# Kernel optimization log

Measured on AMD Instinct MI355X. Metric: run time of the kernel, lower is better.

## Reference

```python
import jax, jax.numpy as jnp
import numpy as np

TEMPERATURE = 8.0  # sqrt(d_k), d_k = 64
MINIMUM_VALUE = -1e9  # stand-in for C.MINIMUM_VALUE


def setup_inputs() -> dict:
    key = jax.random.key(0)
    kq, kk, kv, km = jax.random.split(key, 4)
    B, N, D = 32, 2048, 64
    q = jax.random.normal(kq, (B, N, D), dtype=jnp.float32)
    k = jax.random.normal(kk, (B, N, D), dtype=jnp.float32)
    v = jax.random.normal(kv, (B, N, D), dtype=jnp.float32)
    mask = jax.random.randint(km, (B, N, N), 0, 2, dtype=jnp.int32)
    return {"q": q, "k": k, "v": v, "mask": mask}


def reference(q, k, v, mask):
    # scores: [B, Nq, Nk]
    attn = jnp.einsum("bqd,bkd->bqk", q, k) / TEMPERATURE
    attn = jnp.where(mask > 0, attn, MINIMUM_VALUE)
    attn = jax.nn.softmax(attn, axis=-1)
    # dropout is identity in eval / deterministic reference
    output = jnp.einsum("bqk,bkd->bqd", attn, v)
    return (output, attn)
```

## Files before the change

### kernel.cpp

```cpp
#include <hip/hip_runtime.h>

#define NB 32
#define NN 2048
#define ND 64
#define ROWS 16
#define NBLK (NB * NN / ROWS)

#define LDS_PART 65536
#define LDS_TOTAL 66048

typedef _Float16 half8 __attribute__((ext_vector_type(8)));
typedef float f32x4 __attribute__((ext_vector_type(4)));
typedef int i32x4 __attribute__((ext_vector_type(4)));

union H4 { uint2 u; _Float16 h[4]; };

__device__ __forceinline__ f32x4 mfma16(half8 a, half8 b, f32x4 c) {
    return __builtin_amdgcn_mfma_f32_16x16x32_f16(a, b, c, 0, 0, 0);
}
#define SB() __builtin_amdgcn_sched_barrier(0)
#define LBAR() { asm volatile("s_waitcnt lgkmcnt(0)" ::: "memory"); \
                 __builtin_amdgcn_s_barrier(); \
                 __builtin_amdgcn_sched_barrier(0); }

__global__ __launch_bounds__(256) void cvt_f32_f16_k(const float* __restrict__ src,
                                                     _Float16* __restrict__ dst) {
    int i = blockIdx.x * 256 + threadIdx.x;
    const f32x4* s = (const f32x4*)src;
    f32x4 a = s[2 * i], b = s[2 * i + 1];
    half8 h;
    h[0] = (_Float16)a[0]; h[1] = (_Float16)a[1]; h[2] = (_Float16)a[2]; h[3] = (_Float16)a[3];
    h[4] = (_Float16)b[0]; h[5] = (_Float16)b[1]; h[6] = (_Float16)b[2]; h[7] = (_Float16)b[3];
    ((half8*)dst)[i] = h;
}

__global__ __launch_bounds__(256) void transpose_v_k(const float* __restrict__ v,
                                                     _Float16* __restrict__ vt) {
    __shared__ float tile[64][65];
    int b = blockIdx.x >> 5;
    int k0 = (blockIdx.x & 31) * 64;
    int t = threadIdx.x;
    {
        int dc = t & 15, kr = t >> 4;
        const f32x4* vp = (const f32x4*)(v + ((size_t)(b * NN + k0) * ND));
        #pragma unroll
        for (int i = 0; i < 4; ++i) {
            int kk = kr + i * 16;
            f32x4 x = vp[kk * 16 + dc];
            tile[kk][dc * 4 + 0] = x[0]; tile[kk][dc * 4 + 1] = x[1];
            tile[kk][dc * 4 + 2] = x[2]; tile[kk][dc * 4 + 3] = x[3];
        }
    }
    __syncthreads();
    {
        int d = t >> 2, ks = (t & 3) * 16;
        union { _Float16 hh[16]; uint4 u4[2]; } pk;
        #pragma unroll
        for (int j = 0; j < 16; ++j) pk.hh[j] = (_Float16)tile[ks + j][d];
        uint4* op = (uint4*)(vt + ((size_t)(b * ND + d) * NN + k0 + ks));
        op[0] = pk.u4[0]; op[1] = pk.u4[1];
    }
}

__global__ __launch_bounds__(256) void mask_pack_k(const int* __restrict__ mask,
                                                   unsigned long long* __restrict__ pm) {
    size_t gid = (size_t)blockIdx.x * 256 + threadIdx.x;
    size_t row = gid >> 5;
    int w = ((int)gid >> 2) & 7, lg = (int)gid & 3;
    const i32x4* mp = (const i32x4*)(mask + row * NN + w * 16 + lg * 4);
    unsigned long long bits = 0ull;
    #pragma unroll
    for (int i = 0; i < 16; i += 4) {
        i32x4 m0 = __builtin_nontemporal_load(mp + (size_t)(i + 0) * 32);
        i32x4 m1 = __builtin_nontemporal_load(mp + (size_t)(i + 1) * 32);
        i32x4 m2 = __builtin_nontemporal_load(mp + (size_t)(i + 2) * 32);
        i32x4 m3 = __builtin_nontemporal_load(mp + (size_t)(i + 3) * 32);
        unsigned b0 = (m0[0] > 0 ? 1u : 0u) | (m0[1] > 0 ? 2u : 0u) | (m0[2] > 0 ? 4u : 0u) | (m0[3] > 0 ? 8u : 0u);
        unsigned b1 = (m1[0] > 0 ? 1u : 0u) | (m1[1] > 0 ? 2u : 0u) | (m1[2] > 0 ? 4u : 0u) | (m1[3] > 0 ? 8u : 0u);
        unsigned b2 = (m2[0] > 0 ? 1u : 0u) | (m2[1] > 0 ? 2u : 0u) | (m2[2] > 0 ? 4u : 0u) | (m2[3] > 0 ? 8u : 0u);
        unsigned b3 = (m3[0] > 0 ? 1u : 0u) | (m3[1] > 0 ? 2u : 0u) | (m3[2] > 0 ? 4u : 0u) | (m3[3] > 0 ? 8u : 0u);
        bits |= (unsigned long long)(b0 | (b1 << 4) | (b2 << 8) | (b3 << 12)) << (i * 4);
    }
    pm[gid] = bits;
}

#define LDK(S, base) { \
    const _Float16* kk_ = kp + (size_t)(base) * (128 * ND); \
    S##0a = *(const half8*)(kk_);                S##0b = *(const half8*)(kk_ + 32); \
    S##1a = *(const half8*)(kk_ + 128 * ND);     S##1b = *(const half8*)(kk_ + 128 * ND + 32); \
    S##2a = *(const half8*)(kk_ + 2 * 128 * ND); S##2b = *(const half8*)(kk_ + 2 * 128 * ND + 32); \
    S##3a = *(const half8*)(kk_ + 3 * 128 * ND); S##3b = *(const half8*)(kk_ + 3 * 128 * ND + 32); }

#define CMP1(i, ka_, kb_) { \
    f32x4 acc = {0.f, 0.f, 0.f, 0.f}; \
    acc = mfma16(ka_, qf0, acc); \
    acc = mfma16(kb_, qf1, acc); \
    unsigned mb = (unsigned)(pmask >> ((i) * 4)) & 15u; \
    float e0 = (mb & 1u) ? __expf(acc[0] * 0.125f) : 0.f; \
    float e1 = (mb & 2u) ? __expf(acc[1] * 0.125f) : 0.f; \
    float e2 = (mb & 4u) ? __expf(acc[2] * 0.125f) : 0.f; \
    float e3 = (mb & 8u) ? __expf(acc[3] * 0.125f) : 0.f; \
    rsum += (e0 + e1) + (e2 + e3); \
    H4 y_; y_.h[0] = (_Float16)e0; y_.h[1] = (_Float16)e1; \
    y_.h[2] = (_Float16)e2; y_.h[3] = (_Float16)e3; \
    *(uint2*)(srow + ((((w * 16 + (i) * 128) + lg * 4) * 2) ^ sw)) = y_.u; }

#define CMP4(S, c) { CMP1((c)*4 + 0, S##0a, S##0b) CMP1((c)*4 + 1, S##1a, S##1b) \
                     CMP1((c)*4 + 2, S##2a, S##2b) CMP1((c)*4 + 3, S##3a, S##3b) }

#define LDV(S, base) { \
    const _Float16* vv_ = vp + (size_t)(base) * 32; \
    S##0 = *(const half8*)(vv_);       S##1 = *(const half8*)(vv_ + 32); \
    S##2 = *(const half8*)(vv_ + 64);  S##3 = *(const half8*)(vv_ + 96); \
    S##4 = *(const half8*)(vv_ + 128); S##5 = *(const half8*)(vv_ + 160); \
    S##6 = *(const half8*)(vv_ + 192); S##7 = *(const half8*)(vv_ + 224); }

#define PV1(ks_, vb_) { \
    half8 pa_ = *(const half8*)(pbase + ((((ks_) * 64) + lg * 16) ^ sw)); \
    o = mfma16(pa_, vb_, o); }

#define PV8(S, base) { PV1((base) + 0, S##0) PV1((base) + 1, S##1) \
                       PV1((base) + 2, S##2) PV1((base) + 3, S##3) \
                       PV1((base) + 4, S##4) PV1((base) + 5, S##5) \
                       PV1((base) + 6, S##6) PV1((base) + 7, S##7) }

#define NRM(jj) { \
    int colb_ = l15 * 8 + (jj) * 128; \
    H4 x_; x_.u = *(const uint2*)(s2 + (colb_ ^ sw2)); \
    f32x4 av_; \
    av_[0] = (float)x_.h[0] * linv; av_[1] = (float)x_.h[1] * linv; \
    av_[2] = (float)x_.h[2] * linv; av_[3] = (float)x_.h[3] * linv; \
    *(f32x4*)(arow + (colb_ >> 1)) = av_; }

__global__ __launch_bounds__(512, 4) void attn_main_k(
        const _Float16* __restrict__ qh, const _Float16* __restrict__ kh,
        const _Float16* __restrict__ vtp, const unsigned long long* __restrict__ pm,
        float* __restrict__ outp, float* __restrict__ attnp) {
    extern __shared__ char smem[];

    int bid = blockIdx.x;
    int lin = (bid & 7) * (NBLK / 8) + (bid >> 3);
    int b  = lin >> 7;
    int q0 = (lin & 127) * ROWS;

    int t = threadIdx.x;
    int w = t >> 6, l = t & 63;
    int l15 = l & 15, lg = l >> 4;
    int sw = (l15 & 7) << 4;

    const _Float16* qb = qh + ((size_t)(b * NN + q0 + l15) * ND) + lg * 8;
    half8 qf0 = *(const half8*)(qb);
    half8 qf1 = *(const half8*)(qb + 32);

    unsigned long long pmask = pm[((size_t)(b * NN + q0 + l15) * 8 + w) * 4 + lg];

    const _Float16* kp = kh + (size_t)b * NN * ND + (size_t)(w * 16 + l15) * ND + lg * 8;
    char* srow = smem + l15 * 4096;
    float* part = (float*)(smem + LDS_PART);

    half8 A0a, A0b, A1a, A1b, A2a, A2b, A3a, A3b;
    half8 B0a, B0b, B1a, B1b, B2a, B2b, B3a, B3b;
    float rsum = 0.f;
    LDK(A, 0)  SB();
    LDK(B, 4)  SB();
    CMP4(A, 0) SB();
    LDK(A, 8)  SB();
    CMP4(B, 1) SB();
    LDK(B, 12) SB();
    CMP4(A, 2) SB();
    CMP4(B, 3)

    rsum += __shfl_xor(rsum, 16);
    rsum += __shfl_xor(rsum, 32);
    if (l < 16) part[w * 16 + l] = rsum;
    LBAR();

    if (w < 4) {
        const _Float16* vp = vtp + (size_t)(b * ND + w * 16 + l15) * NN + lg * 8;
        char* pbase = smem + l15 * 4096;
        f32x4 o = {0.f, 0.f, 0.f, 0.f};
        half8 V0, V1, V2, V3, V4, V5, V6, V7;
        half8 W0, W1, W2, W3, W4, W5, W6, W7;
        LDV(V, 0)   SB();
        LDV(W, 8)   SB();
        PV8(V, 0)   SB();
        LDV(V, 16)  SB();
        PV8(W, 8)   SB();
        LDV(W, 24)  SB();
        PV8(V, 16)  SB();
        LDV(V, 32)  SB();
        PV8(W, 24)  SB();
        LDV(W, 40)  SB();
        PV8(V, 32)  SB();
        LDV(V, 48)  SB();
        PV8(W, 40)  SB();
        LDV(W, 56)  SB();
        PV8(V, 48)  SB();
        PV8(W, 56)

        float* ob = outp + ((size_t)(b * NN + q0 + lg * 4)) * ND + w * 16 + l15;
        #pragma unroll
        for (int rr = 0; rr < 4; ++rr) {
            int qr = lg * 4 + rr;
            float s8 = 0.f;
            #pragma unroll
            for (int pw = 0; pw < 8; ++pw) s8 += part[pw * 16 + qr];
            ob[(size_t)rr * ND] = o[rr] / (s8 + 1e-37f);
        }
    } else {
        int r = (w - 4) * 4 + lg;
        float su = 0.f;
        #pragma unroll
        for (int pw = 0; pw < 8; ++pw) su += part[pw * 16 + r];
        float linv = 1.0f / (su + 1e-37f);
        char* s2 = smem + r * 4096;
        int sw2 = (r & 7) << 4;
        float* arow = attnp + ((size_t)(b * NN + q0 + r)) * NN;
        NRM(0)  NRM(1)  NRM(2)  NRM(3)
        NRM(4)  NRM(5)  NRM(6)  NRM(7)
        NRM(8)  NRM(9)  NRM(10) NRM(11)
        NRM(12) NRM(13) NRM(14) NRM(15)
        NRM(16) NRM(17) NRM(18) NRM(19)
        NRM(20) NRM(21) NRM(22) NRM(23)
        NRM(24) NRM(25) NRM(26) NRM(27)
        NRM(28) NRM(29) NRM(30) NRM(31)
    }
}

extern "C" void kernel_launch(void* const* d_in, const int* in_sizes, int n_in,
                              void* d_out, int out_size, void* d_ws, size_t ws_size,
                              hipStream_t stream) {
    const float* q = (const float*)d_in[0];
    const float* k = (const float*)d_in[1];
    const float* v = (const float*)d_in[2];
    const int* mask = (const int*)d_in[3];
    float* outp  = (float*)d_out;
    float* attnp = outp + (size_t)NB * NN * ND;

    _Float16* qh = (_Float16*)d_ws;
    _Float16* kh = qh + (size_t)NB * NN * ND;
    _Float16* vth = kh + (size_t)NB * NN * ND;
    unsigned long long* pm = (unsigned long long*)(vth + (size_t)NB * NN * ND);

    cvt_f32_f16_k<<<2048, 256, 0, stream>>>(q, qh);
    cvt_f32_f16_k<<<2048, 256, 0, stream>>>(k, kh);
    transpose_v_k<<<1024, 256, 0, stream>>>(v, vth);
    mask_pack_k<<<8192, 256, 0, stream>>>(mask, pm);
    attn_main_k<<<NBLK, 512, LDS_TOTAL, stream>>>(qh, kh, vth, pm, outp, attnp);
}
```

Before: 396.5 us.

## Split fused attention into score kernel and output kernel staging fp16 probs in output buffer

The single fused kernel, which held unnormalized fp16 probabilities for 16 rows in 64KB of LDS, is split in two. A score kernel writes the fp16 exp values into the front half of each fp32 attention row in global memory and stores per-row sums. An output kernel then reads them back for the PV matmul and rewrites them in place as normalized fp32. This frees LDS and raises occupancy, but it adds a global write and read of the fp16 score matrix plus an extra launch. In-place correctness depends on the barrier inside each block between the reads and the overwriting writes.

```diff
diff --git a/kernel.cpp b/kernel.cpp
--- a/kernel.cpp
+++ b/kernel.cpp
@@ -4,10 +4,6 @@
 #define NN 2048
 #define ND 64
 #define ROWS 16
-#define NBLK (NB * NN / ROWS)
-
-#define LDS_PART 65536
-#define LDS_TOTAL 66048
 
 typedef _Float16 half8 __attribute__((ext_vector_type(8)));
 typedef float f32x4 __attribute__((ext_vector_type(4)));
@@ -91,7 +87,7 @@
     S##2a = *(const half8*)(kk_ + 2 * 128 * ND); S##2b = *(const half8*)(kk_ + 2 * 128 * ND + 32); \
     S##3a = *(const half8*)(kk_ + 3 * 128 * ND); S##3b = *(const half8*)(kk_ + 3 * 128 * ND + 32); }
 
-#define CMP1(i, ka_, kb_) { \
+#define CMP1A(i, ka_, kb_) { \
     f32x4 acc = {0.f, 0.f, 0.f, 0.f}; \
     acc = mfma16(ka_, qf0, acc); \
     acc = mfma16(kb_, qf1, acc); \
@@ -103,10 +99,48 @@
     rsum += (e0 + e1) + (e2 + e3); \
     H4 y_; y_.h[0] = (_Float16)e0; y_.h[1] = (_Float16)e1; \
     y_.h[2] = (_Float16)e2; y_.h[3] = (_Float16)e3; \
-    *(uint2*)(srow + ((((w * 16 + (i) * 128) + lg * 4) * 2) ^ sw)) = y_.u; }
-
-#define CMP4(S, c) { CMP1((c)*4 + 0, S##0a, S##0b) CMP1((c)*4 + 1, S##1a, S##1b) \
-                     CMP1((c)*4 + 2, S##2a, S##2b) CMP1((c)*4 + 3, S##3a, S##3b) }
+    *(uint2*)(spq + (c * 16 + (i) * 128 + lg * 4)) = y_.u; }
+
+#define CMP4A(S, cc) { CMP1A((cc)*4 + 0, S##0a, S##0b) CMP1A((cc)*4 + 1, S##1a, S##1b) \
+                       CMP1A((cc)*4 + 2, S##2a, S##2b) CMP1A((cc)*4 + 3, S##3a, S##3b) }
+
+__global__ __launch_bounds__(256, 4) void attn_score_k(
+        const _Float16* __restrict__ qh, const _Float16* __restrict__ kh,
+        const unsigned long long* __restrict__ pm,
+        float* __restrict__ attnp, float* __restrict__ rs) {
+    int bid = blockIdx.x;
+    int lin = (bid & 7) * 128 + (bid >> 3);
+    int b = lin >> 5, rg = lin & 31;
+    int t = threadIdx.x, w = t >> 6, l = t & 63;
+    int l15 = l & 15, lg = l >> 4;
+    int row0 = rg * 64 + w * 16;
+    size_t rowg = (size_t)b * NN + row0 + l15;
+
+    const _Float16* qb = qh + rowg * ND + lg * 8;
+    half8 qf0 = *(const half8*)(qb);
+    half8 qf1 = *(const half8*)(qb + 32);
+    _Float16* spq = (_Float16*)((char*)attnp + rowg * ((size_t)NN * 4));
+
+    float rsum = 0.f;
+    #pragma unroll 1
+    for (int c = 0; c < 8; ++c) {
+        unsigned long long pmask = pm[(rowg * 8 + (size_t)c) * 4 + lg];
+        const _Float16* kp = kh + (size_t)b * NN * ND + (size_t)(c * 16 + l15) * ND + lg * 8;
+        half8 A0a, A0b, A1a, A1b, A2a, A2b, A3a, A3b;
+        half8 B0a, B0b, B1a, B1b, B2a, B2b, B3a, B3b;
+        LDK(A, 0)   SB();
+        LDK(B, 4)   SB();
+        CMP4A(A, 0) SB();
+        LDK(A, 8)   SB();
+        CMP4A(B, 1) SB();
+        LDK(B, 12)  SB();
+        CMP4A(A, 2) SB();
+        CMP4A(B, 3) SB();
+    }
+    rsum += __shfl_xor(rsum, 16);
+    rsum += __shfl_xor(rsum, 32);
+    if (l < 16) rs[(size_t)b * NN + row0 + l] = rsum;
+}
 
 #define LDV(S, base) { \
     const _Float16* vv_ = vp + (size_t)(base) * 32; \
@@ -115,115 +149,75 @@
     S##4 = *(const half8*)(vv_ + 128); S##5 = *(const half8*)(vv_ + 160); \
     S##6 = *(const half8*)(vv_ + 192); S##7 = *(const half8*)(vv_ + 224); }
 
-#define PV1(ks_, vb_) { \
-    half8 pa_ = *(const half8*)(pbase + ((((ks_) * 64) + lg * 16) ^ sw)); \
+#define PV1G(ks_, vb_) { \
+    half8 pa_ = *(const half8*)(pap + (size_t)(ks_) * 32); \
     o = mfma16(pa_, vb_, o); }
 
-#define PV8(S, base) { PV1((base) + 0, S##0) PV1((base) + 1, S##1) \
-                       PV1((base) + 2, S##2) PV1((base) + 3, S##3) \
-                       PV1((base) + 4, S##4) PV1((base) + 5, S##5) \
-                       PV1((base) + 6, S##6) PV1((base) + 7, S##7) }
-
-#define NRM(jj) { \
-    int colb_ = l15 * 8 + (jj) * 128; \
-    H4 x_; x_.u = *(const uint2*)(s2 + (colb_ ^ sw2)); \
-    f32x4 av_; \
-    av_[0] = (float)x_.h[0] * linv; av_[1] = (float)x_.h[1] * linv; \
-    av_[2] = (float)x_.h[2] * linv; av_[3] = (float)x_.h[3] * linv; \
-    *(f32x4*)(arow + (colb_ >> 1)) = av_; }
-
-__global__ __launch_bounds__(512, 4) void attn_main_k(
-        const _Float16* __restrict__ qh, const _Float16* __restrict__ kh,
-        const _Float16* __restrict__ vtp, const unsigned long long* __restrict__ pm,
+#define PV8G(S, base) { PV1G((base) + 0, S##0) PV1G((base) + 1, S##1) \
+                        PV1G((base) + 2, S##2) PV1G((base) + 3, S##3) \
+                        PV1G((base) + 4, S##4) PV1G((base) + 5, S##5) \
+                        PV1G((base) + 6, S##6) PV1G((base) + 7, S##7) }
+
+__global__ __launch_bounds__(512, 4) void attn_out_k(
+        const float* __restrict__ rs, const _Float16* __restrict__ vtp,
         float* __restrict__ outp, float* __restrict__ attnp) {
-    extern __shared__ char smem[];
-
     int bid = blockIdx.x;
-    int lin = (bid & 7) * (NBLK / 8) + (bid >> 3);
-    int b  = lin >> 7;
+    int lin = (bid & 7) * 512 + (bid >> 3);
+    int b = lin >> 7;
     int q0 = (lin & 127) * ROWS;
-
-    int t = threadIdx.x;
-    int w = t >> 6, l = t & 63;
+    int t = threadIdx.x, w = t >> 6, l = t & 63;
     int l15 = l & 15, lg = l >> 4;
-    int sw = (l15 & 7) << 4;
-
-    const _Float16* qb = qh + ((size_t)(b * NN + q0 + l15) * ND) + lg * 8;
-    half8 qf0 = *(const half8*)(qb);
-    half8 qf1 = *(const half8*)(qb + 32);
-
-    unsigned long long pmask = pm[((size_t)(b * NN + q0 + l15) * 8 + w) * 4 + lg];
-
-    const _Float16* kp = kh + (size_t)b * NN * ND + (size_t)(w * 16 + l15) * ND + lg * 8;
-    char* srow = smem + l15 * 4096;
-    float* part = (float*)(smem + LDS_PART);
-
-    half8 A0a, A0b, A1a, A1b, A2a, A2b, A3a, A3b;
-    half8 B0a, B0b, B1a, B1b, B2a, B2b, B3a, B3b;
-    float rsum = 0.f;
-    LDK(A, 0)  SB();
-    LDK(B, 4)  SB();
-    CMP4(A, 0) SB();
-    LDK(A, 8)  SB();
-    CMP4(B, 1) SB();
-    LDK(B, 12) SB();
-    CMP4(A, 2) SB();
-    CMP4(B, 3)
-
-    rsum += __shfl_xor(rsum, 16);
-    rsum += __shfl_xor(rsum, 32);
-    if (l < 16) part[w * 16 + l] = rsum;
-    LBAR();
 
     if (w < 4) {
         const _Float16* vp = vtp + (size_t)(b * ND + w * 16 + l15) * NN + lg * 8;
-        char* pbase = smem + l15 * 4096;
+        const _Float16* pap = (const _Float16*)((char*)attnp +
+                              ((size_t)b * NN + q0 + l15) * ((size_t)NN * 4)) + lg * 8;
         f32x4 o = {0.f, 0.f, 0.f, 0.f};
         half8 V0, V1, V2, V3, V4, V5, V6, V7;
         half8 W0, W1, W2, W3, W4, W5, W6, W7;
         LDV(V, 0)   SB();
         LDV(W, 8)   SB();
-        PV8(V, 0)   SB();
+        PV8G(V, 0)  SB();
         LDV(V, 16)  SB();
-        PV8(W, 8)   SB();
+        PV8G(W, 8)  SB();
         LDV(W, 24)  SB();
-        PV8(V, 16)  SB();
+        PV8G(V, 16) SB();
         LDV(V, 32)  SB();
-        PV8(W, 24)  SB();
+        PV8G(W, 24) SB();
         LDV(W, 40)  SB();
-        PV8(V, 32)  SB();
+        PV8G(V, 32) SB();
         LDV(V, 48)  SB();
-        PV8(W, 40)  SB();
+        PV8G(W, 40) SB();
         LDV(W, 56)  SB();
-        PV8(V, 48)  SB();
-        PV8(W, 56)
-
+        PV8G(V, 48) SB();
+        PV8G(W, 56)
+        LBAR();
         float* ob = outp + ((size_t)(b * NN + q0 + lg * 4)) * ND + w * 16 + l15;
         #pragma unroll
         for (int rr = 0; rr < 4; ++rr) {
-            int qr = lg * 4 + rr;
-            float s8 = 0.f;
-            #pragma unroll
-            for (int pw = 0; pw < 8; ++pw) s8 += part[pw * 16 + qr];
+            float s8 = rs[(size_t)b * NN + q0 + lg * 4 + rr];
             ob[(size_t)rr * ND] = o[rr] / (s8 + 1e-37f);
         }
     } else {
         int r = (w - 4) * 4 + lg;
-        float su = 0.f;
-        #pragma unroll
-        for (int pw = 0; pw < 8; ++pw) su += part[pw * 16 + r];
+        size_t rowg = (size_t)b * NN + q0 + r;
+        const _Float16* srow = (const _Float16*)((char*)attnp + rowg * ((size_t)NN * 4));
+        float su = rs[rowg];
         float linv = 1.0f / (su + 1e-37f);
-        char* s2 = smem + r * 4096;
-        int sw2 = (r & 7) << 4;
-        float* arow = attnp + ((size_t)(b * NN + q0 + r)) * NN;
-        NRM(0)  NRM(1)  NRM(2)  NRM(3)
-        NRM(4)  NRM(5)  NRM(6)  NRM(7)
-        NRM(8)  NRM(9)  NRM(10) NRM(11)
-        NRM(12) NRM(13) NRM(14) NRM(15)
-        NRM(16) NRM(17) NRM(18) NRM(19)
-        NRM(20) NRM(21) NRM(22) NRM(23)
-        NRM(24) NRM(25) NRM(26) NRM(27)
-        NRM(28) NRM(29) NRM(30) NRM(31)
+        uint2 xs[32];
+        #pragma unroll
+        for (int c = 0; c < 32; ++c)
+            xs[c] = *(const uint2*)(srow + l15 * 4 + c * 64);
+        LBAR();
+        float* arow = attnp + rowg * NN;
+        #pragma unroll
+        for (int c = 0; c < 32; ++c) {
+            H4 x; x.u = xs[c];
+            f32x4 av;
+            av[0] = (float)x.h[0] * linv; av[1] = (float)x.h[1] * linv;
+            av[2] = (float)x.h[2] * linv; av[3] = (float)x.h[3] * linv;
+            *(f32x4*)(arow + l15 * 4 + c * 64) = av;
+        }
     }
 }
 
@@ -241,10 +235,12 @@
     _Float16* kh = qh + (size_t)NB * NN * ND;
     _Float16* vth = kh + (size_t)NB * NN * ND;
     unsigned long long* pm = (unsigned long long*)(vth + (size_t)NB * NN * ND);
+    float* rs = (float*)(pm + (size_t)NB * NN * 32);
 
     cvt_f32_f16_k<<<2048, 256, 0, stream>>>(q, qh);
     cvt_f32_f16_k<<<2048, 256, 0, stream>>>(k, kh);
     transpose_v_k<<<1024, 256, 0, stream>>>(v, vth);
     mask_pack_k<<<8192, 256, 0, stream>>>(mask, pm);
-    attn_main_k<<<NBLK, 512, LDS_TOTAL, stream>>>(qh, kh, vth, pm, outp, attnp);
-}
+    attn_score_k<<<1024, 256, 0, stream>>>(qh, kh, pm, attnp, rs);
+    attn_out_k<<<4096, 512, 0, stream>>>(rs, vth, outp, attnp);
+}
```

Measured after the change: 691.5 us. +74.4%, slower.
